# Performance work log

Hardware: AMD Instinct MI355X
Metric: run time of the kernel (lower is better)

## Reference

```python
import jax, jax.numpy as jnp
import numpy as np

BLOCK = 32  # block_h == block_w (triton blocksparse requires square blocks)


def setup_inputs() -> dict:
    key = jax.random.key(0)
    kq, kk, kv, kb, km = jax.random.split(key, 5)
    B, H, S, D = 2, 16, 2048, 64
    query = jax.random.normal(kq, (B, H, S, D), dtype=jnp.float32)
    key_t = jax.random.normal(kk, (B, H, S, D), dtype=jnp.float32)
    value = jax.random.normal(kv, (B, H, S, D), dtype=jnp.float32)
    # grouped Conv2d bias (default bias=True, left at random init in the module)
    conv_bias = jax.random.normal(kb, (H,), dtype=jnp.float32)
    mask = jax.random.randint(km, (H, S, S), 0, 2, dtype=jnp.int32)
    return {"query": query, "key": key_t, "value": value,
            "conv_bias": conv_bias, "mask": mask}


def reference(query, key, value, conv_bias, mask):
    # --- build data-dependent block mask (grouped conv, weight==1, stride==kernel==BLOCK) ---
    H, S, _ = mask.shape
    nb = S // BLOCK
    block_sum = mask.reshape(H, nb, BLOCK, nb, BLOCK).sum(axis=(2, 4)).astype(jnp.float32)
    block_mask = (block_sum + conv_bias[:, None, None]) > 0  # [H, nb, nb]

    # element-level allowed pattern: block active AND causal (triton sparse_softmax is_causal=True)
    elem = jnp.repeat(jnp.repeat(block_mask, BLOCK, axis=1), BLOCK, axis=2)  # [H, S, S]
    causal = jnp.tril(jnp.ones((S, S), dtype=bool))
    allow = elem & causal  # [H, S, S]

    # --- sparse SDD: QK^T restricted to active blocks (scale = 1.0) ---
    scores = jnp.einsum('bhsd,bhtd->bhst', query, key)  # [B, H, S, S]

    # --- sparse causal softmax: disallowed positions are -inf; fully-masked rows -> 0 ---
    NEG = jnp.float32(-1e30)
    s = jnp.where(allow[None], scores, NEG)
    m = jnp.max(s, axis=-1, keepdims=True)
    p = jnp.where(allow[None], jnp.exp(s - m), 0.0)
    denom = jnp.sum(p, axis=-1, keepdims=True)
    w = jnp.where(denom > 0, p / denom, 0.0)

    # --- sparse DSD: attention @ V (absent blocks contribute zero) ---
    return jnp.einsum('bhst,bhtd->bhsd', w, value)
```

## Files before the change

kernel.cpp:

```cpp
#include <hip/hip_runtime.h>
#include <hip/hip_bf16.h>


typedef _Float16 f16_t;
typedef f16_t  f16x8  __attribute__((ext_vector_type(8)));
typedef __fp16 fp16x2 __attribute__((ext_vector_type(2)));
typedef float  f32x4  __attribute__((ext_vector_type(4)));
typedef float  f32x16 __attribute__((ext_vector_type(16)));
typedef int    i32x4  __attribute__((ext_vector_type(4)));
typedef int    i32x2  __attribute__((ext_vector_type(2)));
typedef unsigned int u32x4 __attribute__((ext_vector_type(4)));

constexpr int Bc = 2, Hc = 16, Sc = 2048, Dc = 64;
constexpr int NB = Sc / 32;
constexpr float LOG2E = 1.4426950408889634f;
constexpr size_t FRAG_BH = (size_t)NB * 4 * 64 * 8;

__device__ inline f32x16 mfma32(f16x8 a, f16x8 b, f32x16 c) {
    return __builtin_amdgcn_mfma_f32_32x32x16_f16(a, b, c, 0, 0, 0);
}
__device__ inline float fexp2(float x) { return __builtin_amdgcn_exp2f(x); }

union UB { u32x4 u; f16x8 v; };
union PK { fp16x2 h; unsigned int u; };

#if __has_builtin(__builtin_amdgcn_permlane32_swap)
#define HAVE_PLSWAP 1
__device__ inline i32x2 plswap(unsigned int a, unsigned int b) {
    return __builtin_amdgcn_permlane32_swap((int)a, (int)b, false, false);
}
__device__ inline float xhalf_max(float x) {
    i32x2 s = plswap((unsigned int)__float_as_int(x), (unsigned int)__float_as_int(x));
    return fmaxf(__int_as_float(s[0]), __int_as_float(s[1]));
}
__device__ inline float xhalf_sum(float x) {
    i32x2 s = plswap((unsigned int)__float_as_int(x), (unsigned int)__float_as_int(x));
    return __int_as_float(s[0]) + __int_as_float(s[1]);
}
#else
#define HAVE_PLSWAP 0
__device__ inline float xhalf_max(float x) { return fmaxf(x, __shfl_xor(x, 32)); }
__device__ inline float xhalf_sum(float x) { return x + __shfl_xor(x, 32); }
#endif

__global__ __launch_bounds__(256) void k_prep(const float* __restrict__ K,
                                              const float* __restrict__ V,
                                              const int* __restrict__ mask,
                                              const float* __restrict__ bias,
                                              f16_t* __restrict__ khf,
                                              f16_t* __restrict__ vaf,
                                              unsigned char* __restrict__ bm) {
    __shared__ f16_t tile[32 * 66];
    const int bid = blockIdx.x;
    const int t   = threadIdx.x;
    if (bid < 2048) {
        const int bh = bid >> 6, kb = bid & 63;
        const float* src = K + ((size_t)bh * Sc + (size_t)kb * 32) * Dc;
        {
            int r = t >> 3, c8 = (t & 7) * 8;
            f32x4 a = *(const f32x4*)(src + r * Dc + c8);
            f32x4 b = *(const f32x4*)(src + r * Dc + c8 + 4);
            float xs[8] = {a[0], a[1], a[2], a[3], b[0], b[1], b[2], b[3]};
#pragma unroll
            for (int j = 0; j < 8; j++) tile[r * 66 + c8 + j] = (f16_t)xs[j];
        }
        __syncthreads();
        {
            int kc = t >> 6, lane = t & 63, l31 = lane & 31, hi2 = (lane >> 5) & 1;
            f16x8 frag;
#pragma unroll
            for (int j = 0; j < 8; j++)
                frag[j] = tile[l31 * 66 + kc * 16 + hi2 * 8 + j];
            *(f16x8*)(khf + (((size_t)(bh * NB + kb) * 4 + kc) * 64 + lane) * 8) = frag;
        }
    } else if (bid < 4096) {
        const int b2 = bid - 2048;
        const int bh = b2 >> 6, kb = b2 & 63;
        const float* src = V + ((size_t)bh * Sc + (size_t)kb * 32) * Dc;
        {
            int r = t >> 3, c8 = (t & 7) * 8;
            f32x4 a = *(const f32x4*)(src + r * Dc + c8);
            f32x4 b = *(const f32x4*)(src + r * Dc + c8 + 4);
            float xs[8] = {a[0], a[1], a[2], a[3], b[0], b[1], b[2], b[3]};
#pragma unroll
            for (int j = 0; j < 8; j++) tile[r * 66 + c8 + j] = (f16_t)xs[j];
        }
        __syncthreads();
        {
            int f = t >> 6, lane = t & 63, l31 = lane & 31, hi2 = (lane >> 5) & 1;
            int tt = f >> 1, c = f & 1;
            f16x8 frag;
#pragma unroll
            for (int j = 0; j < 8; j++)
                frag[j] = tile[(c * 16 + hi2 * 8 + j) * 66 + tt * 32 + l31];
            *(f16x8*)(vaf + (((size_t)(bh * NB + kb) * 4 + f) * 64 + lane) * 8) = frag;
        }
    } else {
        const int b3 = bid - 4096;
        const int h  = b3 >> 6;
        const int br = b3 & 63;
        float bv = bias[h];
        unsigned char* outp = bm + ((size_t)h * NB + br) * NB;
        if (bv > 0.f) {
            if (t < NB) outp[t] = 1;
            return;
        }
        int bc0 = t >> 3;
        int bc1 = 32 + bc0;
        const int* base = mask + ((size_t)h * Sc + (size_t)br * 32) * (size_t)Sc;
        const int* p0 = base + 4 * t;
        const int* p1 = base + 1024 + 4 * t;
        bool d0 = (bc0 <= br), d1 = (bc1 <= br);
        int acc0 = 0, acc1 = 0;
        if (d0) {
#pragma unroll
            for (int r = 0; r < 4; r++) {
                i32x4 vv = *(const i32x4*)(p0 + (size_t)r * Sc);
                acc0 += vv[0] + vv[1] + vv[2] + vv[3];
            }
        }
        if (d1) {
#pragma unroll
            for (int r = 0; r < 4; r++) {
                i32x4 vv = *(const i32x4*)(p1 + (size_t)r * Sc);
                acc1 += vv[0] + vv[1] + vv[2] + vv[3];
            }
        }
        int g0 = acc0, g1 = acc1;
#pragma unroll
        for (int off = 1; off < 8; off <<= 1) {
            g0 += __shfl_xor(g0, off);
            g1 += __shfl_xor(g1, off);
        }
        bool act0 = (float)g0 + bv > 0.f;
        bool act1 = (float)g1 + bv > 0.f;
        if (d0 && !act0) {
            for (int r = 4; r < 32; r++) {
                i32x4 vv = *(const i32x4*)(p0 + (size_t)r * Sc);
                acc0 += vv[0] + vv[1] + vv[2] + vv[3];
            }
            int s = acc0;
#pragma unroll
            for (int off = 1; off < 8; off <<= 1) s += __shfl_xor(s, off);
            act0 = (float)s + bv > 0.f;
        }
        if (d1 && !act1) {
            for (int r = 4; r < 32; r++) {
                i32x4 vv = *(const i32x4*)(p1 + (size_t)r * Sc);
                acc1 += vv[0] + vv[1] + vv[2] + vv[3];
            }
            int s = acc1;
#pragma unroll
            for (int off = 1; off < 8; off <<= 1) s += __shfl_xor(s, off);
            act1 = (float)s + bv > 0.f;
        }
        if ((t & 7) == 0) {
            if (d0) outp[bc0] = act0 ? 1 : 0;
            if (d1) outp[bc1] = act1 ? 1 : 0;
        }
    }
}

#if HAVE_PLSWAP
#define EXCHANGE_P(PB, B0, B1) do {                                            \
        i32x2 e0_ = plswap(PB[0], PB[2]);                                      \
        i32x2 e1_ = plswap(PB[1], PB[3]);                                      \
        i32x2 e2_ = plswap(PB[4], PB[6]);                                      \
        i32x2 e3_ = plswap(PB[5], PB[7]);                                      \
        B0.u[0] = (unsigned int)e0_[0]; B0.u[1] = (unsigned int)e1_[0];        \
        B0.u[2] = (unsigned int)e0_[1]; B0.u[3] = (unsigned int)e1_[1];        \
        B1.u[0] = (unsigned int)e2_[0]; B1.u[1] = (unsigned int)e3_[0];        \
        B1.u[2] = (unsigned int)e2_[1]; B1.u[3] = (unsigned int)e3_[1];        \
} while (0)
#else
#define EXCHANGE_P(PB, B0, B1) do {                                            \
        unsigned int qb_[8];                                                   \
        _Pragma("unroll")                                                      \
        for (int i_ = 0; i_ < 8; i_++)                                         \
            qb_[i_] = (unsigned int)__shfl_xor((int)PB[i_], 32);               \
        B0.u[0] = hi ? qb_[2] : PB[0]; B0.u[1] = hi ? qb_[3] : PB[1];          \
        B0.u[2] = hi ? PB[2] : qb_[0]; B0.u[3] = hi ? PB[3] : qb_[1];          \
        B1.u[0] = hi ? qb_[6] : PB[4]; B1.u[1] = hi ? qb_[7] : PB[5];          \
        B1.u[2] = hi ? PB[6] : qb_[4]; B1.u[3] = hi ? PB[7] : qb_[5];          \
} while (0)
#endif

#define CORE(OT0, OT1, MR, LR, QH, BROW, kb_) do {                             \
        f32x16 st;                                                             \
        _Pragma("unroll")                                                      \
        for (int r_ = 0; r_ < 16; r_++) st[r_] = 0.f;                          \
        _Pragma("unroll")                                                      \
        for (int kc_ = 0; kc_ < 4; kc_++)                                      \
            st = mfma32(kbuf_[kc_], QH[kc_], st);                              \
        if ((kb_) == (BROW)) {                                                 \
            _Pragma("unroll")                                                  \
            for (int r_ = 0; r_ < 16; r_++) {                                  \
                int kvl_ = (r_ & 3) + 8 * (r_ >> 2) + 4 * hi;                  \
                if (kvl_ > l31) st[r_] = -1e30f;                               \
            }                                                                  \
        }                                                                      \
        float a0_ = fmaxf(fmaxf(st[0], st[1]), st[2]);                         \
        float a1_ = fmaxf(fmaxf(st[3], st[4]), st[5]);                         \
        float a2_ = fmaxf(fmaxf(st[6], st[7]), st[8]);                         \
        float a3_ = fmaxf(fmaxf(st[9], st[10]), st[11]);                       \
        float a4_ = fmaxf(fmaxf(st[12], st[13]), st[14]);                      \
        float b0m_ = fmaxf(fmaxf(a0_, a1_), a2_);                              \
        float b1m_ = fmaxf(fmaxf(a3_, a4_), st[15]);                           \
        float mx_ = xhalf_max(fmaxf(b0m_, b1m_));                              \
        if (__ballot(mx_ > MR + 11.0f)) {                                      \
            float mn_ = fmaxf(MR, mx_);                                        \
            float al_ = fexp2(MR - mn_);                                       \
            MR = mn_;                                                          \
            LR *= al_;                                                         \
            OT0 *= al_; OT1 *= al_;                                            \
        }                                                                      \
        _Pragma("unroll")                                                      \
        for (int r_ = 0; r_ < 16; r_++) st[r_] = fexp2(st[r_] - MR);           \
        {                                                                      \
            float s0 = (st[0] + st[1]) + (st[2] + st[3]);                      \
            float s1 = (st[4] + st[5]) + (st[6] + st[7]);                      \
            float s2 = (st[8] + st[9]) + (st[10] + st[11]);                    \
            float s3 = (st[12] + st[13]) + (st[14] + st[15]);                  \
            LR += ((s0 + s1) + (s2 + s3));                                     \
        }                                                                      \
        unsigned int pb_[8];                                                   \
        _Pragma("unroll")                                                      \
        for (int i_ = 0; i_ < 8; i_++) {                                       \
            PK pk_;                                                            \
            pk_.h = __builtin_amdgcn_cvt_pkrtz(st[2 * i_], st[2 * i_ + 1]);    \
            pb_[i_] = pk_.u;                                                   \
        }                                                                      \
        UB b0_, b1_;                                                           \
        EXCHANGE_P(pb_, b0_, b1_);                                             \
        OT0 = mfma32(va_[0][0], b0_.v, OT0);                                   \
        OT0 = mfma32(va_[0][1], b1_.v, OT0);                                   \
        OT1 = mfma32(va_[1][0], b0_.v, OT1);                                   \
        OT1 = mfma32(va_[1][1], b1_.v, OT1);                                   \
} while (0)

#define QLOAD(QH, q0_) do {                                                    \
        const float* qr_ = q_ptr + (size_t)((q0_) + l31) * Dc + hi * 8;        \
        _Pragma("unroll")                                                      \
        for (int kc_ = 0; kc_ < 4; kc_++) {                                    \
            f32x4 a_ = *(const f32x4*)(qr_ + kc_ * 16);                        \
            f32x4 b_ = *(const f32x4*)(qr_ + kc_ * 16 + 4);                    \
            float xs_[8] = {a_[0], a_[1], a_[2], a_[3], b_[0], b_[1], b_[2], b_[3]}; \
            _Pragma("unroll")                                                  \
            for (int j_ = 0; j_ < 8; j_++) QH[kc_][j_] = (f16_t)(xs_[j_] * LOG2E); \
        }                                                                      \
} while (0)

#define POST(OT0, OT1, MR, LS) do {                                            \
        _Pragma("unroll")                                                      \
        for (int r_ = 0; r_ < 16; r_++) {                                      \
            int d0_ = (r_ & 3) + 8 * (r_ >> 2) + 4 * hi;                       \
            lds_o[d0_ * 33 + l31]        = OT0[r_];                            \
            lds_o[(d0_ + 32) * 33 + l31] = OT1[r_];                            \
        }                                                                      \
        if (hi == 0) { lds_m[l31] = MR; lds_l[l31] = LS; }                     \
} while (0)

#define MERGE_WRITE(OT0, OT1, MR, LS, q0_) do {                                \
        float m1_ = lds_m[l31], l1_ = lds_l[l31];                              \
        float mm_ = fmaxf(MR, m1_);                                            \
        float c0_ = (MR  > -1e37f) ? fexp2(MR  - mm_) : 0.f;                   \
        float c1_ = (m1_ > -1e37f) ? fexp2(m1_ - mm_) : 0.f;                   \
        float lt_ = LS * c0_ + l1_ * c1_;                                      \
        float inv_ = (lt_ > 0.f) ? (1.f / lt_) : 0.f;                          \
        float* op_ = Out + bh_off + (size_t)((q0_) + l31) * Dc;                \
        _Pragma("unroll")                                                      \
        for (int g_ = 0; g_ < 4; g_++) {                                       \
            f32x4 w0_, w1_;                                                    \
            _Pragma("unroll")                                                  \
            for (int jj_ = 0; jj_ < 4; jj_++) {                                \
                int r_ = g_ * 4 + jj_;                                         \
                int d0_ = jj_ + 8 * g_ + 4 * hi;                               \
                w0_[jj_] = (OT0[r_] * c0_ + lds_o[d0_ * 33 + l31] * c1_) * inv_;        \
                w1_[jj_] = (OT1[r_] * c0_ + lds_o[(d0_ + 32) * 33 + l31] * c1_) * inv_; \
            }                                                                  \
            *(f32x4*)(op_ + g_ * 8 + hi * 4)      = w0_;                       \
            *(f32x4*)(op_ + 32 + g_ * 8 + hi * 4) = w1_;                       \
        }                                                                      \
} while (0)

__global__ __launch_bounds__(128, 2) void k_attn(const float* __restrict__ Q,
                                                 const f16_t* __restrict__ KHF,
                                                 const f16_t* __restrict__ VAF,
                                                 const unsigned char* __restrict__ BM,
                                                 float* __restrict__ Out) {
    __shared__ float lds_o[64 * 33];
    __shared__ float lds_m[32];
    __shared__ float lds_l[32];

    const int pair = blockIdx.x >> 5;
    const int bh   = blockIdx.x & 31;
    const int h    = bh & (Hc - 1);
    const int w    = threadIdx.x >> 6;
    const int lane = threadIdx.x & 63;
    const int l31  = lane & 31, hi = lane >> 5;

    const size_t bh_off = (size_t)bh * Sc * Dc;
    const float* q_ptr  = Q + bh_off;
    const f16_t* khfp   = KHF + (size_t)bh * FRAG_BH;
    const f16_t* vafp   = VAF + (size_t)bh * FRAG_BH;

    const int qiA = pair, qiB = 63 - pair;
    const unsigned char* bmA = BM + ((size_t)h * NB + qiA) * NB;
    const unsigned char* bmB = BM + ((size_t)h * NB + qiB) * NB;
    const unsigned long long amA = __ballot(bmA[lane] != 0);
    const unsigned long long amB = __ballot(bmB[lane] != 0);

    f16x8 qhA[4], qhB[4];
    QLOAD(qhA, qiA * 32);
    QLOAD(qhB, qiB * 32);

    f32x16 oA0, oA1, oB0, oB1;
#pragma unroll
    for (int r = 0; r < 16; r++) { oA0[r] = 0.f; oA1[r] = 0.f; oB0[r] = 0.f; oB1[r] = 0.f; }
    float mA = -INFINITY, lA = 0.f, mB = -INFINITY, lB = 0.f;

    for (int kb = w; kb <= qiB; kb += 2) {
        const bool aA = (kb <= qiA) && ((amA >> kb) & 1ull);
        const bool aB = (amB >> kb) & 1ull;
        if (!(aA || aB)) continue;
        f16x8 kbuf_[4];
#pragma unroll
        for (int kc = 0; kc < 4; kc++)
            kbuf_[kc] = *(const f16x8*)(khfp + (((size_t)kb * 4 + kc) * 64 + lane) * 8);
        f16x8 va_[2][2];
#pragma unroll
        for (int t = 0; t < 2; t++)
#pragma unroll
            for (int c = 0; c < 2; c++)
                va_[t][c] = *(const f16x8*)(vafp + (((size_t)kb * 4 + t * 2 + c) * 64 + lane) * 8);
        if (aA) CORE(oA0, oA1, mA, lA, qhA, qiA, kb);
        if (aB) CORE(oB0, oB1, mB, lB, qhB, qiB, kb);
    }

    const float lsA = xhalf_sum(lA);
    const float lsB = xhalf_sum(lB);

    if (w == 1) POST(oA0, oA1, mA, lsA);
    __syncthreads();
    if (w == 0) MERGE_WRITE(oA0, oA1, mA, lsA, qiA * 32);
    __syncthreads();
    if (w == 0) POST(oB0, oB1, mB, lsB);
    __syncthreads();
    if (w == 1) MERGE_WRITE(oB0, oB1, mB, lsB, qiB * 32);
}

extern "C" void kernel_launch(void* const* d_in, const int* in_sizes, int n_in,
                              void* d_out, int out_size, void* d_ws, size_t ws_size,
                              hipStream_t stream) {
    const float* Q    = (const float*)d_in[0];
    const float* K    = (const float*)d_in[1];
    const float* V    = (const float*)d_in[2];
    const float* bias = (const float*)d_in[3];
    const int*   mask = (const int*)d_in[4];
    float* out = (float*)d_out;

    char* ws = (char*)d_ws;
    f16_t* khf = (f16_t*)ws;
    f16_t* vaf = (f16_t*)(ws + (size_t)32 * FRAG_BH * 2);
    unsigned char* bm = (unsigned char*)(ws + (size_t)64 * FRAG_BH * 2);

    k_prep <<<5120, 256, 0, stream>>>(K, V, mask, bias, khf, vaf, bm);
    k_attn <<<Hc * Bc * (NB / 2), 128, 0, stream>>>(Q, khf, vaf, bm, out);
}
```

Baseline: 46.65 us.

## Split paired query blocks into one query block per workgroup, heaviest first

Each workgroup previously handled a pair of query block rows (qi and 63-qi) to balance causal work, sharing K/V fragment loads between them. Now each workgroup handles a single query block row, the grid doubles to 2048 blocks, and blockIdx is mapped so the longest rows launch first. Launch bounds are raised to 4 waves-per-EU occupancy to fit more of the smaller, lower-register workgroups. This trades the K/V load sharing and built-in balance of the pairing for higher occupancy and finer-grained scheduling.

Result: slower. 49.16 us (+5.4%).

```diff
diff --git a/kernel.cpp b/kernel.cpp
--- a/kernel.cpp
+++ b/kernel.cpp
@@ -250,40 +250,7 @@
         }                                                                      \
 } while (0)
 
-#define POST(OT0, OT1, MR, LS) do {                                            \
-        _Pragma("unroll")                                                      \
-        for (int r_ = 0; r_ < 16; r_++) {                                      \
-            int d0_ = (r_ & 3) + 8 * (r_ >> 2) + 4 * hi;                       \
-            lds_o[d0_ * 33 + l31]        = OT0[r_];                            \
-            lds_o[(d0_ + 32) * 33 + l31] = OT1[r_];                            \
-        }                                                                      \
-        if (hi == 0) { lds_m[l31] = MR; lds_l[l31] = LS; }                     \
-} while (0)
-
-#define MERGE_WRITE(OT0, OT1, MR, LS, q0_) do {                                \
-        float m1_ = lds_m[l31], l1_ = lds_l[l31];                              \
-        float mm_ = fmaxf(MR, m1_);                                            \
-        float c0_ = (MR  > -1e37f) ? fexp2(MR  - mm_) : 0.f;                   \
-        float c1_ = (m1_ > -1e37f) ? fexp2(m1_ - mm_) : 0.f;                   \
-        float lt_ = LS * c0_ + l1_ * c1_;                                      \
-        float inv_ = (lt_ > 0.f) ? (1.f / lt_) : 0.f;                          \
-        float* op_ = Out + bh_off + (size_t)((q0_) + l31) * Dc;                \
-        _Pragma("unroll")                                                      \
-        for (int g_ = 0; g_ < 4; g_++) {                                       \
-            f32x4 w0_, w1_;                                                    \
-            _Pragma("unroll")                                                  \
-            for (int jj_ = 0; jj_ < 4; jj_++) {                                \
-                int r_ = g_ * 4 + jj_;                                         \
-                int d0_ = jj_ + 8 * g_ + 4 * hi;                               \
-                w0_[jj_] = (OT0[r_] * c0_ + lds_o[d0_ * 33 + l31] * c1_) * inv_;        \
-                w1_[jj_] = (OT1[r_] * c0_ + lds_o[(d0_ + 32) * 33 + l31] * c1_) * inv_; \
-            }                                                                  \
-            *(f32x4*)(op_ + g_ * 8 + hi * 4)      = w0_;                       \
-            *(f32x4*)(op_ + 32 + g_ * 8 + hi * 4) = w1_;                       \
-        }                                                                      \
-} while (0)
-
-__global__ __launch_bounds__(128, 2) void k_attn(const float* __restrict__ Q,
+__global__ __launch_bounds__(128, 4) void k_attn(const float* __restrict__ Q,
                                                  const f16_t* __restrict__ KHF,
                                                  const f16_t* __restrict__ VAF,
                                                  const unsigned char* __restrict__ BM,
@@ -292,7 +259,7 @@
     __shared__ float lds_m[32];
     __shared__ float lds_l[32];
 
-    const int pair = blockIdx.x >> 5;
+    const int qi   = 63 - (int)(blockIdx.x >> 5);
     const int bh   = blockIdx.x & 31;
     const int h    = bh & (Hc - 1);
     const int w    = threadIdx.x >> 6;
@@ -304,25 +271,21 @@
     const f16_t* khfp   = KHF + (size_t)bh * FRAG_BH;
     const f16_t* vafp   = VAF + (size_t)bh * FRAG_BH;
 
-    const int qiA = pair, qiB = 63 - pair;
-    const unsigned char* bmA = BM + ((size_t)h * NB + qiA) * NB;
-    const unsigned char* bmB = BM + ((size_t)h * NB + qiB) * NB;
-    const unsigned long long amA = __ballot(bmA[lane] != 0);
-    const unsigned long long amB = __ballot(bmB[lane] != 0);
-
-    f16x8 qhA[4], qhB[4];
-    QLOAD(qhA, qiA * 32);
-    QLOAD(qhB, qiB * 32);
-
-    f32x16 oA0, oA1, oB0, oB1;
-#pragma unroll
-    for (int r = 0; r < 16; r++) { oA0[r] = 0.f; oA1[r] = 0.f; oB0[r] = 0.f; oB1[r] = 0.f; }
-    float mA = -INFINITY, lA = 0.f, mB = -INFINITY, lB = 0.f;
-
-    for (int kb = w; kb <= qiB; kb += 2) {
-        const bool aA = (kb <= qiA) && ((amA >> kb) & 1ull);
-        const bool aB = (amB >> kb) & 1ull;
-        if (!(aA || aB)) continue;
+    const int q0   = qi * 32;
+    const int brow = qi;
+    const unsigned char* bmrow = BM + ((size_t)h * NB + brow) * NB;
+    const unsigned long long actmask = __ballot(bmrow[lane] != 0);
+
+    f16x8 qh[4];
+    QLOAD(qh, q0);
+
+    f32x16 ot0, ot1;
+#pragma unroll
+    for (int r = 0; r < 16; r++) { ot0[r] = 0.f; ot1[r] = 0.f; }
+    float mrow = -INFINITY, lrow = 0.f;
+
+    for (int kb = w; kb <= brow; kb += 2) {
+        if (!((actmask >> kb) & 1ull)) continue;
         f16x8 kbuf_[4];
 #pragma unroll
         for (int kc = 0; kc < 4; kc++)
@@ -333,20 +296,42 @@
 #pragma unroll
             for (int c = 0; c < 2; c++)
                 va_[t][c] = *(const f16x8*)(vafp + (((size_t)kb * 4 + t * 2 + c) * 64 + lane) * 8);
-        if (aA) CORE(oA0, oA1, mA, lA, qhA, qiA, kb);
-        if (aB) CORE(oB0, oB1, mB, lB, qhB, qiB, kb);
+        CORE(ot0, ot1, mrow, lrow, qh, brow, kb);
     }
 
-    const float lsA = xhalf_sum(lA);
-    const float lsB = xhalf_sum(lB);
-
-    if (w == 1) POST(oA0, oA1, mA, lsA);
+    float lsum = xhalf_sum(lrow);
+    if (w == 1) {
+#pragma unroll
+        for (int r = 0; r < 16; r++) {
+            int d0 = (r & 3) + 8 * (r >> 2) + 4 * hi;
+            lds_o[d0 * 33 + l31]        = ot0[r];
+            lds_o[(d0 + 32) * 33 + l31] = ot1[r];
+        }
+        if (hi == 0) { lds_m[l31] = mrow; lds_l[l31] = lsum; }
+    }
     __syncthreads();
-    if (w == 0) MERGE_WRITE(oA0, oA1, mA, lsA, qiA * 32);
-    __syncthreads();
-    if (w == 0) POST(oB0, oB1, mB, lsB);
-    __syncthreads();
-    if (w == 1) MERGE_WRITE(oB0, oB1, mB, lsB, qiB * 32);
+    if (w == 0) {
+        float m1 = lds_m[l31], l1 = lds_l[l31];
+        float mm = fmaxf(mrow, m1);
+        float a0 = (mrow > -1e37f) ? fexp2(mrow - mm) : 0.f;
+        float a1 = (m1   > -1e37f) ? fexp2(m1   - mm) : 0.f;
+        float lt = lsum * a0 + l1 * a1;
+        float inv = (lt > 0.f) ? (1.f / lt) : 0.f;
+        float* op = Out + bh_off + (size_t)(q0 + l31) * Dc;
+#pragma unroll
+        for (int g = 0; g < 4; g++) {
+            f32x4 w0, w1;
+#pragma unroll
+            for (int jj = 0; jj < 4; jj++) {
+                int r = g * 4 + jj;
+                int d0 = jj + 8 * g + 4 * hi;
+                w0[jj] = (ot0[r] * a0 + lds_o[d0 * 33 + l31] * a1) * inv;
+                w1[jj] = (ot1[r] * a0 + lds_o[(d0 + 32) * 33 + l31] * a1) * inv;
+            }
+            *(f32x4*)(op + g * 8 + hi * 4)      = w0;
+            *(f32x4*)(op + 32 + g * 8 + hi * 4) = w1;
+        }
+    }
 }
 
 extern "C" void kernel_launch(void* const* d_in, const int* in_sizes, int n_in,
@@ -365,5 +350,5 @@
     unsigned char* bm = (unsigned char*)(ws + (size_t)64 * FRAG_BH * 2);
 
     k_prep <<<5120, 256, 0, stream>>>(K, V, mask, bias, khf, vaf, bm);
-    k_attn <<<Hc * Bc * (NB / 2), 128, 0, stream>>>(Q, khf, vaf, bm, out);
-}
+    k_attn <<<Bc * Hc * NB, 128, 0, stream>>>(Q, khf, vaf, bm, out);
+}
```
